# Kernel optimization log

Hardware: AMD Instinct MI355X
Metric: run time of the kernel (lower is better)

The kernel has to match this reference:

```python
import jax, jax.numpy as jnp
import numpy as np

CODEBOOK_SIZE = 1024
EMBED_DIM = 256
X_SHAPE = (8, 4, 32, 32, EMBED_DIM)  # [B, T, H, W, C] video latents


def setup_inputs() -> dict:
    key = jax.random.key(0)
    kx, kc = jax.random.split(key)
    x = jax.random.normal(kx, X_SHAPE, dtype=jnp.float32)
    # variance_scaling(scale=1.0, mode='fan_in', distribution='uniform') over (codebook_size, d):
    # fan_in = d, limit = sqrt(3 / fan_in)
    limit = float(np.sqrt(3.0 / EMBED_DIM))
    codebook = jax.random.uniform(kc, (CODEBOOK_SIZE, EMBED_DIM), dtype=jnp.float32,
                                  minval=-limit, maxval=limit)
    return {"x": x, "codebook": codebook}


def reference(x, codebook):
    d = x.shape[-1]
    k = codebook.shape[0]
    flat = x.reshape(-1, d)  # [N, d]
    distances = (jnp.sum(flat * flat, axis=-1, keepdims=True)
                 - 2.0 * jnp.dot(flat, codebook.T)
                 + jnp.sum(codebook * codebook, axis=-1))
    distances = distances.reshape(x.shape[:-1] + (k,))
    encoding_indices = jnp.argmin(distances, axis=-1)  # [...]
    encodings = jax.nn.one_hot(encoding_indices, k, dtype=x.dtype)  # [..., K]
    # quantize: one-hot @ codebook (== gather of codebook rows)
    quantized = jnp.dot(encodings, codebook)  # [..., d]
    return quantized
```

## Files before the change

kernel.cpp:

```cpp
#include <hip/hip_runtime.h>


#define D         256
#define K_TOTAL   1024
#define N_ROWS    32768
#define TM        64
#define TN        64
#define NCHUNK    (K_TOTAL / TN)
#define CS_STRIDE 260

__global__ void norms_kernel(const float* __restrict__ x, const float* __restrict__ cb,
                             float* __restrict__ xnorm, float* __restrict__ cnorm) {
    const int wave = threadIdx.x >> 6;
    const int lane = threadIdx.x & 63;
    const int row  = blockIdx.x * 4 + wave;

    const float* src;
    float* dst;
    int idx;
    if (row < N_ROWS) { src = x  + (size_t)row * D;             dst = xnorm; idx = row; }
    else              { src = cb + (size_t)(row - N_ROWS) * D;  dst = cnorm; idx = row - N_ROWS; }

    float4 v = *(const float4*)(src + lane * 4);
    float sx = v.x * v.x;
    float sy = v.y * v.y;
    float sz = v.z * v.z;
    float sw = v.w * v.w;
    double s = (double)sx + (double)sy + (double)sz + (double)sw;
    #pragma unroll
    for (int off = 32; off > 0; off >>= 1)
        s += __shfl_down(s, off, 64);
    if (lane == 0) dst[idx] = (float)s;
}

__global__ __launch_bounds__(256, 2)
void vq_kernel(const float* __restrict__ x, const float* __restrict__ cb,
               const float* __restrict__ xnorm, const float* __restrict__ cnorm,
               float* __restrict__ out) {
    __shared__ float cs[TN * CS_STRIDE];
    __shared__ float red_val[TM * 16];
    __shared__ int   red_idx[TM * 16];
    __shared__ int   best_idx[TM];

    const int tid = threadIdx.x;
    const int tx  = tid & 15;
    const int ty  = tid >> 4;
    const int n0  = blockIdx.x * TM;

    float runmin[4];
    int   runidx[4];
    float S[4];
    const float* xrow[4];
    #pragma unroll
    for (int i = 0; i < 4; ++i) {
        runmin[i] = 1e30f; runidx[i] = 0;
        const int n = n0 + ty + 16 * i;
        S[i]    = xnorm[n];
        xrow[i] = x + (size_t)n * D;
    }

    for (int kc = 0; kc < NCHUNK; ++kc) {
        const int k0 = kc * TN;

        __syncthreads();
        {
            const int col4 = tid & 63;
            const int row  = tid >> 6;
            #pragma unroll
            for (int r = 0; r < 16; ++r) {
                const int rr = row + 4 * r;
                float4 v = *(const float4*)(cb + (size_t)(k0 + rr) * D + col4 * 4);
                *(float4*)(cs + rr * CS_STRIDE + col4 * 4) = v;
            }
        }
        __syncthreads();

        float acc[4][4];
        #pragma unroll
        for (int i = 0; i < 4; ++i)
            #pragma unroll
            for (int j = 0; j < 4; ++j) acc[i][j] = 0.f;

        #pragma unroll 2
        for (int dd = 0; dd < D; dd += 4) {
            float4 a[4], b[4];
            #pragma unroll
            for (int i = 0; i < 4; ++i) a[i] = *(const float4*)(xrow[i] + dd);
            #pragma unroll
            for (int j = 0; j < 4; ++j) b[j] = *(const float4*)(cs + (tx + 16 * j) * CS_STRIDE + dd);
            #pragma unroll
            for (int i = 0; i < 4; ++i)
                #pragma unroll
                for (int j = 0; j < 4; ++j) {
                    acc[i][j] += a[i].x * b[j].x;
                    acc[i][j] += a[i].y * b[j].y;
                    acc[i][j] += a[i].z * b[j].z;
                    acc[i][j] += a[i].w * b[j].w;
                }
        }

        #pragma unroll
        for (int j = 0; j < 4; ++j) {
            const int k = k0 + tx + 16 * j;
            const float cn = cnorm[k];
            #pragma unroll
            for (int i = 0; i < 4; ++i) {
                const float t = S[i] - 2.0f * acc[i][j];
                const float q = t + cn;
                if (q < runmin[i]) { runmin[i] = q; runidx[i] = k; }
            }
        }
    }

    __syncthreads();
    #pragma unroll
    for (int i = 0; i < 4; ++i) {
        const int row = ty + 16 * i;
        red_val[row * 16 + tx] = runmin[i];
        red_idx[row * 16 + tx] = runidx[i];
    }
    __syncthreads();
    if (tid < TM) {
        const int row = tid;
        float bv = red_val[row * 16];
        int   bi = red_idx[row * 16];
        #pragma unroll
        for (int t = 1; t < 16; ++t) {
            const float v = red_val[row * 16 + t];
            const int  ix = red_idx[row * 16 + t];
            if (v < bv || (v == bv && ix < bi)) { bv = v; bi = ix; }
        }
        best_idx[row] = bi;
    }
    __syncthreads();

    {
        const int col4 = tid & 63;
        const int row  = tid >> 6;
        #pragma unroll
        for (int r = 0; r < 16; ++r) {
            const int rr = row + 4 * r;
            const int k  = best_idx[rr];
            float4 v = *(const float4*)(cb + (size_t)k * D + col4 * 4);
            *(float4*)(out + (size_t)(n0 + rr) * D + col4 * 4) = v;
        }
    }
}

extern "C" void kernel_launch(void* const* d_in, const int* in_sizes, int n_in,
                              void* d_out, int out_size, void* d_ws, size_t ws_size,
                              hipStream_t stream) {
    const float* x  = (const float*)d_in[0];
    const float* cb = (const float*)d_in[1];
    float* out = (float*)d_out;

    float* xnorm = (float*)d_ws;
    float* cnorm = xnorm + N_ROWS;

    norms_kernel<<<(N_ROWS + K_TOTAL) / 4, 256, 0, stream>>>(x, cb, xnorm, cnorm);
    vq_kernel<<<N_ROWS / TM, 256, 0, stream>>>(x, cb, xnorm, cnorm, out);
}
```

Measured before the change: 374.0 us.

## Stage x tile in LDS, prefetch codebook chunks via registers, use 512 threads

After: 497.3 us. 33.0% more time.

```diff
diff --git a/kernel.cpp b/kernel.cpp
--- a/kernel.cpp
+++ b/kernel.cpp
@@ -8,35 +8,72 @@
 #define TN        64
 #define NCHUNK    (K_TOTAL / TN)
 #define CS_STRIDE 260
+#define NTHREADS  512
+#define NI        2
+#define NJ        4
 
 __global__ void norms_kernel(const float* __restrict__ x, const float* __restrict__ cb,
                              float* __restrict__ xnorm, float* __restrict__ cnorm) {
     const int wave = threadIdx.x >> 6;
     const int lane = threadIdx.x & 63;
-    const int row  = blockIdx.x * 4 + wave;
-
-    const float* src;
-    float* dst;
-    int idx;
-    if (row < N_ROWS) { src = x  + (size_t)row * D;             dst = xnorm; idx = row; }
-    else              { src = cb + (size_t)(row - N_ROWS) * D;  dst = cnorm; idx = row - N_ROWS; }
-
-    float4 v = *(const float4*)(src + lane * 4);
-    float sx = v.x * v.x;
-    float sy = v.y * v.y;
-    float sz = v.z * v.z;
-    float sw = v.w * v.w;
-    double s = (double)sx + (double)sy + (double)sz + (double)sw;
-    #pragma unroll
-    for (int off = 32; off > 0; off >>= 1)
-        s += __shfl_down(s, off, 64);
-    if (lane == 0) dst[idx] = (float)s;
+    const int row0 = (blockIdx.x * 4 + wave) * 4;
+
+    double s[4];
+    #pragma unroll
+    for (int r = 0; r < 4; ++r) {
+        const int row = row0 + r;
+        const float* src = (row < N_ROWS) ? (x + (size_t)row * D)
+                                          : (cb + (size_t)(row - N_ROWS) * D);
+        float4 v = *(const float4*)(src + lane * 4);
+        float sx = v.x * v.x;
+        float sy = v.y * v.y;
+        float sz = v.z * v.z;
+        float sw = v.w * v.w;
+        s[r] = (double)sx + (double)sy + (double)sz + (double)sw;
+    }
+    #pragma unroll
+    for (int off = 32; off > 0; off >>= 1) {
+        #pragma unroll
+        for (int r = 0; r < 4; ++r) s[r] += __shfl_down(s[r], off, 64);
+    }
+    if (lane == 0) {
+        #pragma unroll
+        for (int r = 0; r < 4; ++r) {
+            const int row = row0 + r;
+            if (row < N_ROWS) xnorm[row] = (float)s[r];
+            else              cnorm[row - N_ROWS] = (float)s[r];
+        }
+    }
 }
 
-__global__ __launch_bounds__(256, 2)
+
+#define LOAD_G(aR, bR, ddv) do {                                               \
+    _Pragma("unroll")                                                          \
+    for (int i_ = 0; i_ < NI; ++i_)                                            \
+        aR[i_] = *(const float4*)(xs + (ty + 32 * i_) * CS_STRIDE + (ddv));    \
+    _Pragma("unroll")                                                          \
+    for (int j_ = 0; j_ < NJ; ++j_)                                            \
+        bR[j_] = *(const float4*)(cs + (tx + 16 * j_) * CS_STRIDE + (ddv));    \
+} while (0)
+
+#define FMA_G(aR, bR) do {                                                     \
+    _Pragma("unroll")                                                          \
+    for (int i_ = 0; i_ < NI; ++i_) {                                          \
+        _Pragma("unroll")                                                      \
+        for (int j_ = 0; j_ < NJ; ++j_) {                                      \
+            acc[i_][j_] += aR[i_].x * bR[j_].x;                                \
+            acc[i_][j_] += aR[i_].y * bR[j_].y;                                \
+            acc[i_][j_] += aR[i_].z * bR[j_].z;                                \
+            acc[i_][j_] += aR[i_].w * bR[j_].w;                                \
+        }                                                                      \
+    }                                                                          \
+} while (0)
+
+__global__ __launch_bounds__(NTHREADS, 2)
 void vq_kernel(const float* __restrict__ x, const float* __restrict__ cb,
                const float* __restrict__ xnorm, const float* __restrict__ cnorm,
                float* __restrict__ out) {
+    __shared__ float xs[TM * CS_STRIDE];
     __shared__ float cs[TN * CS_STRIDE];
     __shared__ float red_val[TM * 16];
     __shared__ int   red_idx[TM * 16];
@@ -47,75 +84,101 @@
     const int ty  = tid >> 4;
     const int n0  = blockIdx.x * TM;
 
-    float runmin[4];
-    int   runidx[4];
-    float S[4];
-    const float* xrow[4];
-    #pragma unroll
-    for (int i = 0; i < 4; ++i) {
+    const int col4 = tid & 63;
+    const int rowp = tid >> 6;
+
+    #pragma unroll
+    for (int r = 0; r < 8; ++r) {
+        const int rr = rowp + 8 * r;
+        float4 v = *(const float4*)(x + (size_t)(n0 + rr) * D + col4 * 4);
+        *(float4*)(xs + rr * CS_STRIDE + col4 * 4) = v;
+    }
+    #pragma unroll
+    for (int r = 0; r < 8; ++r) {
+        const int rr = rowp + 8 * r;
+        float4 v = *(const float4*)(cb + (size_t)rr * D + col4 * 4);
+        *(float4*)(cs + rr * CS_STRIDE + col4 * 4) = v;
+    }
+
+    float runmin[NI];
+    int   runidx[NI];
+    float S[NI];
+    #pragma unroll
+    for (int i = 0; i < NI; ++i) {
         runmin[i] = 1e30f; runidx[i] = 0;
-        const int n = n0 + ty + 16 * i;
-        S[i]    = xnorm[n];
-        xrow[i] = x + (size_t)n * D;
-    }
+        S[i] = xnorm[n0 + ty + 32 * i];
+    }
+    __syncthreads();
 
     for (int kc = 0; kc < NCHUNK; ++kc) {
         const int k0 = kc * TN;
 
-        __syncthreads();
-        {
-            const int col4 = tid & 63;
-            const int row  = tid >> 6;
-            #pragma unroll
-            for (int r = 0; r < 16; ++r) {
-                const int rr = row + 4 * r;
-                float4 v = *(const float4*)(cb + (size_t)(k0 + rr) * D + col4 * 4);
-                *(float4*)(cs + rr * CS_STRIDE + col4 * 4) = v;
+        float4 sreg[8];
+        if (kc + 1 < NCHUNK) {
+            const int kn = k0 + TN;
+            #pragma unroll
+            for (int r = 0; r < 8; ++r) {
+                const int rr = rowp + 8 * r;
+                sreg[r] = *(const float4*)(cb + (size_t)(kn + rr) * D + col4 * 4);
             }
         }
-        __syncthreads();
-
-        float acc[4][4];
-        #pragma unroll
-        for (int i = 0; i < 4; ++i)
-            #pragma unroll
-            for (int j = 0; j < 4; ++j) acc[i][j] = 0.f;
-
-        #pragma unroll 2
-        for (int dd = 0; dd < D; dd += 4) {
-            float4 a[4], b[4];
-            #pragma unroll
-            for (int i = 0; i < 4; ++i) a[i] = *(const float4*)(xrow[i] + dd);
-            #pragma unroll
-            for (int j = 0; j < 4; ++j) b[j] = *(const float4*)(cs + (tx + 16 * j) * CS_STRIDE + dd);
-            #pragma unroll
-            for (int i = 0; i < 4; ++i)
-                #pragma unroll
-                for (int j = 0; j < 4; ++j) {
-                    acc[i][j] += a[i].x * b[j].x;
-                    acc[i][j] += a[i].y * b[j].y;
-                    acc[i][j] += a[i].z * b[j].z;
-                    acc[i][j] += a[i].w * b[j].w;
-                }
-        }
-
-        #pragma unroll
-        for (int j = 0; j < 4; ++j) {
+        float cn[NJ];
+        #pragma unroll
+        for (int j = 0; j < NJ; ++j) cn[j] = cnorm[k0 + tx + 16 * j];
+
+        float acc[NI][NJ];
+        #pragma unroll
+        for (int i = 0; i < NI; ++i)
+            #pragma unroll
+            for (int j = 0; j < NJ; ++j) acc[i][j] = 0.f;
+
+        float4 aA[NI], bA[NJ], aB[NI], bB[NJ], aC[NI], bC[NJ], aD[NI], bD[NJ];
+        LOAD_G(aA, bA, 0);
+        LOAD_G(aB, bB, 4);
+        #pragma unroll 1
+        for (int it = 0; it < 15; ++it) {
+            const int base = it * 16;
+            LOAD_G(aC, bC, base + 8);
+            FMA_G(aA, bA);
+            LOAD_G(aD, bD, base + 12);
+            FMA_G(aB, bB);
+            LOAD_G(aA, bA, base + 16);
+            FMA_G(aC, bC);
+            LOAD_G(aB, bB, base + 20);
+            FMA_G(aD, bD);
+        }
+        LOAD_G(aC, bC, 248);
+        FMA_G(aA, bA);
+        LOAD_G(aD, bD, 252);
+        FMA_G(aB, bB);
+        FMA_G(aC, bC);
+        FMA_G(aD, bD);
+
+        #pragma unroll
+        for (int j = 0; j < NJ; ++j) {
             const int k = k0 + tx + 16 * j;
-            const float cn = cnorm[k];
-            #pragma unroll
-            for (int i = 0; i < 4; ++i) {
+            #pragma unroll
+            for (int i = 0; i < NI; ++i) {
                 const float t = S[i] - 2.0f * acc[i][j];
-                const float q = t + cn;
+                const float q = t + cn[j];
                 if (q < runmin[i]) { runmin[i] = q; runidx[i] = k; }
             }
         }
-    }
-
-    __syncthreads();
-    #pragma unroll
-    for (int i = 0; i < 4; ++i) {
-        const int row = ty + 16 * i;
+
+        __syncthreads();
+        if (kc + 1 < NCHUNK) {
+            #pragma unroll
+            for (int r = 0; r < 8; ++r) {
+                const int rr = rowp + 8 * r;
+                *(float4*)(cs + rr * CS_STRIDE + col4 * 4) = sreg[r];
+            }
+            __syncthreads();
+        }
+    }
+
+    #pragma unroll
+    for (int i = 0; i < NI; ++i) {
+        const int row = ty + 32 * i;
         red_val[row * 16 + tx] = runmin[i];
         red_idx[row * 16 + tx] = runidx[i];
     }
@@ -135,11 +198,9 @@
     __syncthreads();
 
     {
-        const int col4 = tid & 63;
-        const int row  = tid >> 6;
-        #pragma unroll
-        for (int r = 0; r < 16; ++r) {
-            const int rr = row + 4 * r;
+        #pragma unroll
+        for (int r = 0; r < 8; ++r) {
+            const int rr = rowp + 8 * r;
             const int k  = best_idx[rr];
             float4 v = *(const float4*)(cb + (size_t)k * D + col4 * 4);
             *(float4*)(out + (size_t)(n0 + rr) * D + col4 * 4) = v;
@@ -157,6 +218,6 @@
     float* xnorm = (float*)d_ws;
     float* cnorm = xnorm + N_ROWS;
 
-    norms_kernel<<<(N_ROWS + K_TOTAL) / 4, 256, 0, stream>>>(x, cb, xnorm, cnorm);
-    vq_kernel<<<N_ROWS / TM, 256, 0, stream>>>(x, cb, xnorm, cnorm, out);
+    norms_kernel<<<(N_ROWS + K_TOTAL) / 16, 256, 0, stream>>>(x, cb, xnorm, cnorm);
+    vq_kernel<<<N_ROWS / TM, NTHREADS, 0, stream>>>(x, cb, xnorm, cnorm, out);
 }
```
